# Kernel tuning notes

Hardware: AMD Instinct MI355X
Metric: run time of the kernel (lower is better)

The kernel has to match this reference:

```python
import jax, jax.numpy as jnp
import numpy as np

N, E, H, T = 50000, 100000, 512, 6  # nodes, edges, hidden_size, num_edge_types


def setup_inputs() -> dict:
    key = jax.random.key(0)
    ks = jax.random.split(key, 14)
    xav = 1.0 / np.sqrt(H)
    return {
        "statement_embeddings": jax.random.normal(ks[0], (N, H), jnp.float32),
        "source_indices": jax.random.randint(ks[1], (E,), 0, N, dtype=jnp.int32),
        "dest_indices": jax.random.randint(ks[2], (E,), 0, N, dtype=jnp.int32),
        "edge_types": jax.random.randint(ks[3], (E,), 0, T, dtype=jnp.int32),
        "num_nodes": N,
        "hidden_size": H,
        # edge_dense: Dense(features=6*H), xavier_uniform kernel, tiny-normal bias
        "W_edge": jax.random.uniform(ks[4], (H, T * H), jnp.float32, -1.0, 1.0) * np.sqrt(6.0 / (H + T * H)),
        "b_edge": jax.random.normal(ks[5], (T * H,), jnp.float32) * 1e-6,
        # GRUCell params (flax convention: input denses have bias; hidden r/z denses no bias; hidden n dense has bias)
        "W_ir": jax.random.normal(ks[6], (H, H), jnp.float32) * xav,
        "W_iz": jax.random.normal(ks[7], (H, H), jnp.float32) * xav,
        "W_in": jax.random.normal(ks[8], (H, H), jnp.float32) * xav,
        "b_ir": jnp.zeros((H,), jnp.float32),
        "b_iz": jnp.zeros((H,), jnp.float32),
        "b_in": jnp.zeros((H,), jnp.float32),
        "W_hr": jax.random.normal(ks[9], (H, H), jnp.float32) * xav,
        "W_hz": jax.random.normal(ks[10], (H, H), jnp.float32) * xav,
        "W_hn": jax.random.normal(ks[11], (H, H), jnp.float32) * xav,
        "b_hn": jnp.zeros((H,), jnp.float32),
    }


def reference(statement_embeddings, source_indices, dest_indices, edge_types,
              num_nodes, hidden_size,
              W_edge, b_edge,
              W_ir, W_iz, W_in, b_ir, b_iz, b_in,
              W_hr, W_hz, W_hn, b_hn):
    num_edge_types = 6
    # gather source node embeddings: [E, H]
    src = statement_embeddings[source_indices]
    # per-edge dense to all edge types: [E, T*H] -> [E, T, H]
    all_types = (src @ W_edge + b_edge).reshape(-1, num_edge_types, hidden_size)
    # select the slice for each edge's type: [E, H]
    msgs = jnp.take_along_axis(all_types, edge_types[:, None, None], axis=1)[:, 0, :]
    # scatter-add to destination nodes: [N, H]
    proposed = jax.ops.segment_sum(msgs, dest_indices, num_segments=num_nodes)
    # GRU update: inputs=proposed, carry=statement_embeddings
    h = statement_embeddings
    r = jax.nn.sigmoid(proposed @ W_ir + b_ir + h @ W_hr)
    z = jax.nn.sigmoid(proposed @ W_iz + b_iz + h @ W_hz)
    n = jnp.tanh(proposed @ W_in + b_in + r * (h @ W_hn + b_hn))
    return (1.0 - z) * n + z * h
```

## Files before the change

kernel.cpp:

```cpp
#include <hip/hip_runtime.h>
#include <hip/hip_bf16.h>
#include <math.h>

#define H 512
#define NT 6
#define BM 64
#define BN 64
#define BK 32
#define LDW (BK + 8)

typedef short bf16x8 __attribute__((ext_vector_type(8)));
typedef float f32x4 __attribute__((ext_vector_type(4)));

__device__ __forceinline__ float sigmoidf_(float x) { return 1.0f / (1.0f + expf(-x)); }

__device__ __forceinline__ unsigned short f2bf(float f) {
    unsigned int u = __float_as_uint(f);
    u = (u + 0x7FFF + ((u >> 16) & 1)) >> 16;
    return (unsigned short)u;
}

__global__ void hist_kernel(const int* __restrict__ etype, int E, int* __restrict__ meta) {
    __shared__ int lh[NT];
    if (threadIdx.x < NT) lh[threadIdx.x] = 0;
    __syncthreads();
    int i = blockIdx.x * blockDim.x + threadIdx.x;
    if (i < E) atomicAdd(&lh[etype[i]], 1);
    __syncthreads();
    if (threadIdx.x < NT) {
        int c = lh[threadIdx.x];
        if (c) atomicAdd(&meta[threadIdx.x], c);
    }
}

__global__ void prefix_kernel(int* __restrict__ meta) {
    if (threadIdx.x == 0 && blockIdx.x == 0) {
        int acc = 0;
        for (int t = 0; t < NT; ++t) {
            meta[8 + t]  = acc;
            meta[16 + t] = acc;
            acc += ((meta[t] + BM - 1) / BM) * BM;
        }
        meta[8 + NT] = acc;
    }
}

__global__ void scatter_perm_kernel(const int* __restrict__ etype, int E,
                                    int* __restrict__ meta, int* __restrict__ perm) {
    __shared__ int lcount[NT];
    __shared__ int lbase[NT];
    const int tid = threadIdx.x;
    if (tid < NT) lcount[tid] = 0;
    __syncthreads();
    int i = blockIdx.x * blockDim.x + tid;
    int t = 0, rank = 0;
    if (i < E) {
        t = etype[i];
        rank = atomicAdd(&lcount[t], 1);
    }
    __syncthreads();
    if (tid < NT) {
        int c = lcount[tid];
        lbase[tid] = c ? atomicAdd(&meta[16 + tid], c) : 0;
    }
    __syncthreads();
    if (i < E) perm[lbase[t] + rank] = i;
}

__global__ void conv_bf16_kernel(const float* __restrict__ in, unsigned short* __restrict__ out, int n4) {
    int i = blockIdx.x * blockDim.x + threadIdx.x;
    if (i < n4) {
        float4 v = ((const float4*)in)[i];
        ushort4 o;
        o.x = f2bf(v.x); o.y = f2bf(v.y); o.z = f2bf(v.z); o.w = f2bf(v.w);
        ((ushort4*)out)[i] = o;
    }
}

__global__ void conv_gru_w_kernel(const float* __restrict__ Wir, const float* __restrict__ Wiz,
                                  const float* __restrict__ Win, const float* __restrict__ Whr,
                                  const float* __restrict__ Whz, const float* __restrict__ Whn,
                                  unsigned short* __restrict__ Brt, unsigned short* __restrict__ Bzt,
                                  unsigned short* __restrict__ Bnit, unsigned short* __restrict__ Bnht) {
    int idx = blockIdx.x * blockDim.x + threadIdx.x;
    if (idx >= 512 * 1024) return;
    int n = idx >> 10;
    int k = idx & 1023;
    int kk = k & 511;
    const float* wr = (k < 512) ? Wir : Whr;
    const float* wz = (k < 512) ? Wiz : Whz;
    Brt[idx] = f2bf(wr[kk * H + n]);
    Bzt[idx] = f2bf(wz[kk * H + n]);
    if (k < 512) Bnit[n * H + k]  = f2bf(Win[k * H + n]);
    else         Bnht[n * H + kk] = f2bf(Whn[kk * H + n]);
}

__global__ void conv_edge_w_kernel(const float* __restrict__ W_edge, unsigned short* __restrict__ WeT) {
    int idx = blockIdx.x * blockDim.x + threadIdx.x;
    if (idx >= 3072 * 512) return;
    int n = idx >> 9;
    int k = idx & 511;
    WeT[idx] = f2bf(W_edge[(size_t)k * (NT * H) + n]);
}

__global__ __launch_bounds__(256)
void edge_msg_mfma(const unsigned short* __restrict__ emb_bf,
                   const int* __restrict__ src_idx,
                   const int* __restrict__ dst_idx,
                   const float* __restrict__ b_edge,
                   const unsigned short* __restrict__ WeT,
                   const int* __restrict__ meta,
                   const int* __restrict__ perm,
                   float* __restrict__ proposed)
{
    __shared__ short As[BM][LDW];
    __shared__ short Bs[BN][LDW];
    __shared__ int ls_src[BM];
    __shared__ int ls_dst[BM];

    const int rowBase = blockIdx.y * BM;
    if (rowBase >= meta[8 + NT]) return;
    int t = 0;
    while (rowBase >= meta[8 + t + 1]) ++t;

    const int colBase = blockIdx.x * BN;
    const int tid = threadIdx.x;

    if (tid < BM) {
        int e = perm[rowBase + tid];
        int s = -1, d = -1;
        if (e >= 0) { s = src_idx[e] * H; d = dst_idx[e] * H; }
        ls_src[tid] = s;
        ls_dst[tid] = d;
    }
    __syncthreads();

    const int sRow = tid >> 2;
    const int sK   = (tid & 3) * 8;
    const int lane = tid & 63;
    const int wave = tid >> 6;
    const int wm = (wave >> 1) * 32;
    const int wn = (wave & 1) * 32;
    const int q = lane >> 4;
    const int r = lane & 15;

    f32x4 acc[2][2];
    #pragma unroll
    for (int i = 0; i < 2; ++i)
        #pragma unroll
        for (int j = 0; j < 2; ++j) acc[i][j] = (f32x4){0.f, 0.f, 0.f, 0.f};

    const int sA = ls_src[sRow];
    const size_t bRowBase = ((size_t)(t * H + colBase + sRow)) * H;

    for (int k0 = 0; k0 < H; k0 += BK) {
        uint4 av = make_uint4(0, 0, 0, 0);
        if (sA >= 0) av = *(const uint4*)&emb_bf[(size_t)sA + k0 + sK];
        *(uint4*)&As[sRow][sK] = av;
        *(uint4*)&Bs[sRow][sK] = *(const uint4*)&WeT[bRowBase + k0 + sK];
        __syncthreads();
        #pragma unroll
        for (int i = 0; i < 2; ++i) {
            bf16x8 a = *(const bf16x8*)&As[wm + i * 16 + r][q * 8];
            #pragma unroll
            for (int j = 0; j < 2; ++j) {
                bf16x8 b = *(const bf16x8*)&Bs[wn + j * 16 + r][q * 8];
                acc[i][j] = __builtin_amdgcn_mfma_f32_16x16x32_bf16(a, b, acc[i][j], 0, 0, 0);
            }
        }
        __syncthreads();
    }

    #pragma unroll
    for (int i = 0; i < 2; ++i) {
        #pragma unroll
        for (int reg = 0; reg < 4; ++reg) {
            int rowL = wm + i * 16 + q * 4 + reg;
            int d = ls_dst[rowL];
            if (d < 0) continue;
            #pragma unroll
            for (int j = 0; j < 2; ++j) {
                int col = colBase + wn + j * 16 + r;
                atomicAdd(&proposed[(size_t)d + col], acc[i][j][reg] + b_edge[t * H + col]);
            }
        }
    }
}

__global__ __launch_bounds__(256)
void gru_mfma(const unsigned short* __restrict__ prop_bf,
              const unsigned short* __restrict__ emb_bf,
              const float* __restrict__ emb_f32,
              const unsigned short* __restrict__ Brt,
              const unsigned short* __restrict__ Bzt,
              const unsigned short* __restrict__ Bnit,
              const unsigned short* __restrict__ Bnht,
              const float* __restrict__ bir, const float* __restrict__ biz,
              const float* __restrict__ bin, const float* __restrict__ bhn,
              float* __restrict__ out, int N)
{
    __shared__ short As[BM][LDW];
    __shared__ short Brs[BN][LDW];
    __shared__ short Bzs[BN][LDW];
    __shared__ short Bns[BN][LDW];

    const int rowBase = blockIdx.y * BM;
    const int colBase = blockIdx.x * BN;
    const int tid = threadIdx.x;
    const int sRow = tid >> 2;
    const int sK   = (tid & 3) * 8;
    const int lane = tid & 63;
    const int wave = tid >> 6;
    const int wm = (wave >> 1) * 32;
    const int wn = (wave & 1) * 32;
    const int q = lane >> 4;
    const int r = lane & 15;

    const int aRow = rowBase + sRow;
    const bool aValid = aRow < N;

    f32x4 accR[2][2], accZ[2][2], accNI[2][2], accNH[2][2];
    #pragma unroll
    for (int i = 0; i < 2; ++i)
        #pragma unroll
        for (int j = 0; j < 2; ++j) {
            accR[i][j] = (f32x4){0.f, 0.f, 0.f, 0.f};
            accZ[i][j] = accR[i][j];
            accNI[i][j] = accR[i][j];
            accNH[i][j] = accR[i][j];
        }

    const size_t bRow = (size_t)(colBase + sRow);

    for (int k0 = 0; k0 < 2 * H; k0 += BK) {
        const bool half = (k0 >= H);
        const int kk = half ? (k0 - H) : k0;
        const unsigned short* Asrc = half ? emb_bf : prop_bf;
        uint4 av = make_uint4(0, 0, 0, 0);
        if (aValid) av = *(const uint4*)&Asrc[(size_t)aRow * H + kk + sK];
        *(uint4*)&As[sRow][sK] = av;
        *(uint4*)&Brs[sRow][sK] = *(const uint4*)&Brt[bRow * 1024 + k0 + sK];
        *(uint4*)&Bzs[sRow][sK] = *(const uint4*)&Bzt[bRow * 1024 + k0 + sK];
        const unsigned short* Bn = half ? Bnht : Bnit;
        *(uint4*)&Bns[sRow][sK] = *(const uint4*)&Bn[bRow * H + kk + sK];
        __syncthreads();

        #pragma unroll
        for (int i = 0; i < 2; ++i) {
            bf16x8 a = *(const bf16x8*)&As[wm + i * 16 + r][q * 8];
            #pragma unroll
            for (int j = 0; j < 2; ++j) {
                bf16x8 br = *(const bf16x8*)&Brs[wn + j * 16 + r][q * 8];
                bf16x8 bz = *(const bf16x8*)&Bzs[wn + j * 16 + r][q * 8];
                bf16x8 bn = *(const bf16x8*)&Bns[wn + j * 16 + r][q * 8];
                accR[i][j] = __builtin_amdgcn_mfma_f32_16x16x32_bf16(a, br, accR[i][j], 0, 0, 0);
                accZ[i][j] = __builtin_amdgcn_mfma_f32_16x16x32_bf16(a, bz, accZ[i][j], 0, 0, 0);
                if (half) accNH[i][j] = __builtin_amdgcn_mfma_f32_16x16x32_bf16(a, bn, accNH[i][j], 0, 0, 0);
                else      accNI[i][j] = __builtin_amdgcn_mfma_f32_16x16x32_bf16(a, bn, accNI[i][j], 0, 0, 0);
            }
        }
        __syncthreads();
    }

    #pragma unroll
    for (int i = 0; i < 2; ++i) {
        #pragma unroll
        for (int reg = 0; reg < 4; ++reg) {
            int row = rowBase + wm + i * 16 + q * 4 + reg;
            if (row >= N) continue;
            #pragma unroll
            for (int j = 0; j < 2; ++j) {
                int col = colBase + wn + j * 16 + r;
                float rg = sigmoidf_(accR[i][j][reg] + bir[col]);
                float zg = sigmoidf_(accZ[i][j][reg] + biz[col]);
                float ng = tanhf(accNI[i][j][reg] + bin[col] + rg * (accNH[i][j][reg] + bhn[col]));
                float h = emb_f32[(size_t)row * H + col];
                out[(size_t)row * H + col] = (1.0f - zg) * ng + zg * h;
            }
        }
    }
}

extern "C" void kernel_launch(void* const* d_in, const int* in_sizes, int n_in,
                              void* d_out, int out_size, void* d_ws, size_t ws_size,
                              hipStream_t stream) {
    const float* emb     = (const float*)d_in[0];
    const int*   src_idx = (const int*)d_in[1];
    const int*   dst_idx = (const int*)d_in[2];
    const int*   etype   = (const int*)d_in[3];
    const float* W_edge  = (const float*)d_in[6];
    const float* b_edge  = (const float*)d_in[7];
    const float* Wir = (const float*)d_in[8];
    const float* Wiz = (const float*)d_in[9];
    const float* Win = (const float*)d_in[10];
    const float* bir = (const float*)d_in[11];
    const float* biz = (const float*)d_in[12];
    const float* bin = (const float*)d_in[13];
    const float* Whr = (const float*)d_in[14];
    const float* Whz = (const float*)d_in[15];
    const float* Whn = (const float*)d_in[16];
    const float* bhn = (const float*)d_in[17];

    const int E = in_sizes[1];
    const int N = in_sizes[0] / H;
    const int NH = N * H;

    char* ws = (char*)d_ws;
    float*          proposed = (float*)ws;                       ws += (size_t)NH * 4;
    unsigned short* prop_bf  = (unsigned short*)ws;              ws += (size_t)NH * 2;
    unsigned short* emb_bf   = (unsigned short*)ws;              ws += (size_t)NH * 2;
    unsigned short* Brt      = (unsigned short*)ws;              ws += 512 * 1024 * 2;
    unsigned short* Bzt      = (unsigned short*)ws;              ws += 512 * 1024 * 2;
    unsigned short* Bnit     = (unsigned short*)ws;              ws += 512 * 512 * 2;
    unsigned short* Bnht     = (unsigned short*)ws;              ws += 512 * 512 * 2;
    unsigned short* WeT      = (unsigned short*)ws;              ws += 3072 * 512 * 2;
    int*            meta     = (int*)ws;                         ws += 32 * 4;
    int*            perm     = (int*)ws;
    const int maxRowTiles = (E + BM - 1) / BM + NT;

    hipMemsetAsync(proposed, 0, (size_t)NH * 4, stream);
    hipMemsetAsync(meta, 0, 32 * 4, stream);
    hipMemsetAsync(perm, 0xFF, (size_t)maxRowTiles * BM * 4, stream);

    const int n4 = NH / 4;
    conv_bf16_kernel<<<(n4 + 255) / 256, 256, 0, stream>>>(emb, emb_bf, n4);
    conv_gru_w_kernel<<<(512 * 1024 + 255) / 256, 256, 0, stream>>>(
        Wir, Wiz, Win, Whr, Whz, Whn, Brt, Bzt, Bnit, Bnht);
    conv_edge_w_kernel<<<(3072 * 512 + 255) / 256, 256, 0, stream>>>(W_edge, WeT);

    hist_kernel<<<(E + 255) / 256, 256, 0, stream>>>(etype, E, meta);
    prefix_kernel<<<1, 64, 0, stream>>>(meta);
    scatter_perm_kernel<<<(E + 255) / 256, 256, 0, stream>>>(etype, E, meta, perm);

    dim3 egrid(H / BN, maxRowTiles);
    edge_msg_mfma<<<egrid, 256, 0, stream>>>(emb_bf, src_idx, dst_idx, b_edge, WeT,
                                             meta, perm, proposed);

    conv_bf16_kernel<<<(n4 + 255) / 256, 256, 0, stream>>>(proposed, prop_bf, n4);

    dim3 ggrid(H / BN, (N + BM - 1) / BM);
    gru_mfma<<<ggrid, 256, 0, stream>>>(prop_bf, emb_bf, emb, Brt, Bzt, Bnit, Bnht,
                                        bir, biz, bin, bhn, (float*)d_out, N);
}
```

Baseline: 912.3 us.

## Replace atomic scatter with CSR segment reduce and async LDS loads in GEMMs

Builds a destination-sorted CSR layout (node histogram, multi-pass scan, slot assignment) so each edge message is written as bf16 to a unique slot. A segment-reduce kernel then sums messages per node directly into bf16, replacing the fp32 atomic scatter and the separate conversion pass. Both MFMA GEMMs now stage tiles with global_load_lds async copies in a per-wave fragment layout, loading a full 64-row block per k-step. This adds a large E×H message buffer, several extra small launches, and bf16 rounding of messages. The GRU kernel no longer bounds-checks rows when loading A, so it can read past the end when N is not a multiple of 64.

```diff
diff --git a/kernel.cpp b/kernel.cpp
--- a/kernel.cpp
+++ b/kernel.cpp
@@ -6,8 +6,6 @@
 #define NT 6
 #define BM 64
 #define BN 64
-#define BK 32
-#define LDW (BK + 8)
 
 typedef short bf16x8 __attribute__((ext_vector_type(8)));
 typedef float f32x4 __attribute__((ext_vector_type(4)));
@@ -18,6 +16,15 @@
     unsigned int u = __float_as_uint(f);
     u = (u + 0x7FFF + ((u >> 16) & 1)) >> 16;
     return (unsigned short)u;
+}
+__device__ __forceinline__ float bf2f(unsigned short s) {
+    unsigned int u = ((unsigned int)s) << 16;
+    return __uint_as_float(u);
+}
+
+__device__ __forceinline__ void async16(const unsigned short* g, short* l) {
+    __builtin_amdgcn_global_load_lds((const __attribute__((address_space(1))) void*)g,
+                                     (__attribute__((address_space(3))) void*)l, 16, 0, 0);
 }
 
 __global__ void hist_kernel(const int* __restrict__ etype, int E, int* __restrict__ meta) {
@@ -65,6 +72,59 @@
     }
     __syncthreads();
     if (i < E) perm[lbase[t] + rank] = i;
+}
+
+__global__ void node_hist_kernel(const int* __restrict__ dst, int E, int* __restrict__ cnt) {
+    int i = blockIdx.x * blockDim.x + threadIdx.x;
+    if (i < E) atomicAdd(&cnt[dst[i]], 1);
+}
+
+__global__ void scan1_kernel(const int* __restrict__ cnt, int n,
+                             int* __restrict__ nodeStart, int* __restrict__ partials) {
+    __shared__ int sh[256];
+    const int tid = threadIdx.x;
+    const int base = blockIdx.x * 1024 + tid * 4;
+    int v[4];
+    int tsum = 0;
+    #pragma unroll
+    for (int j = 0; j < 4; ++j) { v[j] = (base + j < n) ? cnt[base + j] : 0; tsum += v[j]; }
+    sh[tid] = tsum;
+    __syncthreads();
+    for (int ofs = 1; ofs < 256; ofs <<= 1) {
+        int add = (tid >= ofs) ? sh[tid - ofs] : 0;
+        __syncthreads();
+        sh[tid] += add;
+        __syncthreads();
+    }
+    int run = sh[tid] - tsum;
+    #pragma unroll
+    for (int j = 0; j < 4; ++j) {
+        if (base + j < n) nodeStart[base + j] = run;
+        run += v[j];
+    }
+    if (tid == 255) partials[blockIdx.x] = sh[255];
+}
+
+__global__ void scan2_kernel(int* __restrict__ partials, int nB, int* __restrict__ nodeStart, int n) {
+    if (threadIdx.x == 0 && blockIdx.x == 0) {
+        int acc = 0;
+        for (int b = 0; b < nB; ++b) { int t = partials[b]; partials[b] = acc; acc += t; }
+        nodeStart[n] = acc;
+    }
+}
+
+__global__ void scan3_kernel(int* __restrict__ nodeStart, const int* __restrict__ partials, int n) {
+    int i = blockIdx.x * blockDim.x + threadIdx.x;
+    if (i < n) nodeStart[i] += partials[i >> 10];
+}
+
+__global__ void slot_kernel(const int* __restrict__ dst, int E, const int* __restrict__ nodeStart,
+                            int* __restrict__ cursor, int* __restrict__ destSlot) {
+    int i = blockIdx.x * blockDim.x + threadIdx.x;
+    if (i < E) {
+        int d = dst[i];
+        destSlot[i] = nodeStart[d] + atomicAdd(&cursor[d], 1);
+    }
 }
 
 __global__ void conv_bf16_kernel(const float* __restrict__ in, unsigned short* __restrict__ out, int n4) {
@@ -104,19 +164,19 @@
 }
 
 __global__ __launch_bounds__(256)
-void edge_msg_mfma(const unsigned short* __restrict__ emb_bf,
-                   const int* __restrict__ src_idx,
-                   const int* __restrict__ dst_idx,
-                   const float* __restrict__ b_edge,
-                   const unsigned short* __restrict__ WeT,
-                   const int* __restrict__ meta,
-                   const int* __restrict__ perm,
-                   float* __restrict__ proposed)
+void edge_msg_mfma2(const unsigned short* __restrict__ emb_bf,
+                    const int* __restrict__ src_idx,
+                    const float* __restrict__ b_edge,
+                    const unsigned short* __restrict__ WeT,
+                    const int* __restrict__ meta,
+                    const int* __restrict__ perm,
+                    const int* __restrict__ destSlot,
+                    unsigned short* __restrict__ msgbuf)
 {
-    __shared__ short As[BM][LDW];
-    __shared__ short Bs[BN][LDW];
-    __shared__ int ls_src[BM];
-    __shared__ int ls_dst[BM];
+    __shared__ __align__(16) short lds[8 * 512];
+    __shared__ __align__(16) short Cs[64][72];
+    __shared__ int ls_slot[BM];
+    __shared__ int ls_srcb[BM];
 
     const int rowBase = blockIdx.y * BM;
     if (rowBase >= meta[8 + NT]) return;
@@ -125,24 +185,29 @@
 
     const int colBase = blockIdx.x * BN;
     const int tid = threadIdx.x;
-
     if (tid < BM) {
         int e = perm[rowBase + tid];
-        int s = -1, d = -1;
-        if (e >= 0) { s = src_idx[e] * H; d = dst_idx[e] * H; }
-        ls_src[tid] = s;
-        ls_dst[tid] = d;
-    }
-    __syncthreads();
-
-    const int sRow = tid >> 2;
-    const int sK   = (tid & 3) * 8;
+        ls_slot[tid] = (e >= 0) ? destSlot[e] : -1;
+        ls_srcb[tid] = (e >= 0) ? src_idx[e] * H : 0;
+    }
+    __syncthreads();
+
     const int lane = tid & 63;
-    const int wave = tid >> 6;
-    const int wm = (wave >> 1) * 32;
-    const int wn = (wave & 1) * 32;
+    const int wv = tid >> 6;
+    const int r = lane & 15;
     const int q = lane >> 4;
-    const int r = lane & 15;
+    const int wm = (wv >> 1) * 32;
+    const int wn = (wv & 1) * 32;
+
+    const unsigned short* pg[2];
+    #pragma unroll
+    for (int s = 0; s < 2; ++s) {
+        int grp = wv * 2 + s;
+        if (grp < 4) pg[s] = emb_bf + (size_t)ls_srcb[grp * 16 + r] + q * 8;
+        else         pg[s] = WeT + ((size_t)(t * H + colBase + (grp - 4) * 16 + r)) * H + q * 8;
+    }
+    short* ld0 = &lds[(wv * 2) * 512];
+    short* ld1 = &lds[(wv * 2 + 1) * 512];
 
     f32x4 acc[2][2];
     #pragma unroll
@@ -150,74 +215,88 @@
         #pragma unroll
         for (int j = 0; j < 2; ++j) acc[i][j] = (f32x4){0.f, 0.f, 0.f, 0.f};
 
-    const int sA = ls_src[sRow];
-    const size_t bRowBase = ((size_t)(t * H + colBase + sRow)) * H;
-
-    for (int k0 = 0; k0 < H; k0 += BK) {
-        uint4 av = make_uint4(0, 0, 0, 0);
-        if (sA >= 0) av = *(const uint4*)&emb_bf[(size_t)sA + k0 + sK];
-        *(uint4*)&As[sRow][sK] = av;
-        *(uint4*)&Bs[sRow][sK] = *(const uint4*)&WeT[bRowBase + k0 + sK];
+    for (int ks = 0; ks < 16; ++ks) {
+        async16(pg[0], ld0);
+        async16(pg[1], ld1);
+        pg[0] += 32; pg[1] += 32;
         __syncthreads();
-        #pragma unroll
-        for (int i = 0; i < 2; ++i) {
-            bf16x8 a = *(const bf16x8*)&As[wm + i * 16 + r][q * 8];
-            #pragma unroll
-            for (int j = 0; j < 2; ++j) {
-                bf16x8 b = *(const bf16x8*)&Bs[wn + j * 16 + r][q * 8];
-                acc[i][j] = __builtin_amdgcn_mfma_f32_16x16x32_bf16(a, b, acc[i][j], 0, 0, 0);
-            }
-        }
+        bf16x8 a0 = *(const bf16x8*)&lds[(wm / 16 + 0) * 512 + lane * 8];
+        bf16x8 a1 = *(const bf16x8*)&lds[(wm / 16 + 1) * 512 + lane * 8];
+        bf16x8 b0 = *(const bf16x8*)&lds[(4 + wn / 16 + 0) * 512 + lane * 8];
+        bf16x8 b1 = *(const bf16x8*)&lds[(4 + wn / 16 + 1) * 512 + lane * 8];
+        acc[0][0] = __builtin_amdgcn_mfma_f32_16x16x32_bf16(a0, b0, acc[0][0], 0, 0, 0);
+        acc[0][1] = __builtin_amdgcn_mfma_f32_16x16x32_bf16(a0, b1, acc[0][1], 0, 0, 0);
+        acc[1][0] = __builtin_amdgcn_mfma_f32_16x16x32_bf16(a1, b0, acc[1][0], 0, 0, 0);
+        acc[1][1] = __builtin_amdgcn_mfma_f32_16x16x32_bf16(a1, b1, acc[1][1], 0, 0, 0);
         __syncthreads();
     }
 
-    #pragma unroll
-    for (int i = 0; i < 2; ++i) {
+    float bias0 = b_edge[t * H + colBase + wn + r];
+    float bias1 = b_edge[t * H + colBase + wn + 16 + r];
+    #pragma unroll
+    for (int i = 0; i < 2; ++i)
         #pragma unroll
         for (int reg = 0; reg < 4; ++reg) {
-            int rowL = wm + i * 16 + q * 4 + reg;
-            int d = ls_dst[rowL];
-            if (d < 0) continue;
-            #pragma unroll
-            for (int j = 0; j < 2; ++j) {
-                int col = colBase + wn + j * 16 + r;
-                atomicAdd(&proposed[(size_t)d + col], acc[i][j][reg] + b_edge[t * H + col]);
-            }
-        }
-    }
+            int row = wm + i * 16 + q * 4 + reg;
+            Cs[row][wn + r]      = (short)f2bf(acc[i][0][reg] + bias0);
+            Cs[row][wn + 16 + r] = (short)f2bf(acc[i][1][reg] + bias1);
+        }
+    __syncthreads();
+
+    int row = tid >> 2;
+    int cc = (tid & 3) * 16;
+    int slot = ls_slot[row];
+    if (slot >= 0) {
+        uint4* dst0 = (uint4*)&msgbuf[(size_t)slot * H + colBase + cc];
+        dst0[0] = *(const uint4*)&Cs[row][cc];
+        dst0[1] = *(const uint4*)&Cs[row][cc + 8];
+    }
+}
+
+__global__ void segreduce_kernel(const unsigned short* __restrict__ msgbuf,
+                                 const int* __restrict__ nodeStart,
+                                 unsigned short* __restrict__ prop_bf, int N) {
+    int idx = blockIdx.x * blockDim.x + threadIdx.x;
+    if (idx >= N * 64) return;
+    int node = idx >> 6;
+    int cg = (idx & 63) * 8;
+    int s0 = nodeStart[node], s1 = nodeStart[node + 1];
+    float acc[8] = {0.f, 0.f, 0.f, 0.f, 0.f, 0.f, 0.f, 0.f};
+    for (int s = s0; s < s1; ++s) {
+        uint4 v = *(const uint4*)&msgbuf[(size_t)s * H + cg];
+        const unsigned short* u = (const unsigned short*)&v;
+        #pragma unroll
+        for (int j = 0; j < 8; ++j) acc[j] += bf2f(u[j]);
+    }
+    unsigned short o[8];
+    #pragma unroll
+    for (int j = 0; j < 8; ++j) o[j] = f2bf(acc[j]);
+    *(uint4*)&prop_bf[(size_t)node * H + cg] = *(const uint4*)o;
 }
 
 __global__ __launch_bounds__(256)
-void gru_mfma(const unsigned short* __restrict__ prop_bf,
-              const unsigned short* __restrict__ emb_bf,
-              const float* __restrict__ emb_f32,
-              const unsigned short* __restrict__ Brt,
-              const unsigned short* __restrict__ Bzt,
-              const unsigned short* __restrict__ Bnit,
-              const unsigned short* __restrict__ Bnht,
-              const float* __restrict__ bir, const float* __restrict__ biz,
-              const float* __restrict__ bin, const float* __restrict__ bhn,
-              float* __restrict__ out, int N)
+void gru_mfma2(const unsigned short* __restrict__ prop_bf,
+               const unsigned short* __restrict__ emb_bf,
+               const float* __restrict__ emb_f32,
+               const unsigned short* __restrict__ Brt,
+               const unsigned short* __restrict__ Bzt,
+               const unsigned short* __restrict__ Bnit,
+               const unsigned short* __restrict__ Bnht,
+               const float* __restrict__ bir, const float* __restrict__ biz,
+               const float* __restrict__ bin, const float* __restrict__ bhn,
+               float* __restrict__ out, int N)
 {
-    __shared__ short As[BM][LDW];
-    __shared__ short Brs[BN][LDW];
-    __shared__ short Bzs[BN][LDW];
-    __shared__ short Bns[BN][LDW];
-
+    __shared__ __align__(16) short lds[4 * 2048];
+
+    const int tid = threadIdx.x;
+    const int lane = tid & 63;
+    const int wv = tid >> 6;
+    const int r = lane & 15;
+    const int q = lane >> 4;
     const int rowBase = blockIdx.y * BM;
     const int colBase = blockIdx.x * BN;
-    const int tid = threadIdx.x;
-    const int sRow = tid >> 2;
-    const int sK   = (tid & 3) * 8;
-    const int lane = tid & 63;
-    const int wave = tid >> 6;
-    const int wm = (wave >> 1) * 32;
-    const int wn = (wave & 1) * 32;
-    const int q = lane >> 4;
-    const int r = lane & 15;
-
-    const int aRow = rowBase + sRow;
-    const bool aValid = aRow < N;
+    const int wm = (wv >> 1) * 32;
+    const int wn = (wv & 1) * 32;
 
     f32x4 accR[2][2], accZ[2][2], accNI[2][2], accNH[2][2];
     #pragma unroll
@@ -230,36 +309,63 @@
             accNH[i][j] = accR[i][j];
         }
 
-    const size_t bRow = (size_t)(colBase + sRow);
-
-    for (int k0 = 0; k0 < 2 * H; k0 += BK) {
-        const bool half = (k0 >= H);
-        const int kk = half ? (k0 - H) : k0;
-        const unsigned short* Asrc = half ? emb_bf : prop_bf;
-        uint4 av = make_uint4(0, 0, 0, 0);
-        if (aValid) av = *(const uint4*)&Asrc[(size_t)aRow * H + kk + sK];
-        *(uint4*)&As[sRow][sK] = av;
-        *(uint4*)&Brs[sRow][sK] = *(const uint4*)&Brt[bRow * 1024 + k0 + sK];
-        *(uint4*)&Bzs[sRow][sK] = *(const uint4*)&Bzt[bRow * 1024 + k0 + sK];
-        const unsigned short* Bn = half ? Bnht : Bnit;
-        *(uint4*)&Bns[sRow][sK] = *(const uint4*)&Bn[bRow * H + kk + sK];
-        __syncthreads();
-
-        #pragma unroll
-        for (int i = 0; i < 2; ++i) {
-            bf16x8 a = *(const bf16x8*)&As[wm + i * 16 + r][q * 8];
-            #pragma unroll
-            for (int j = 0; j < 2; ++j) {
-                bf16x8 br = *(const bf16x8*)&Brs[wn + j * 16 + r][q * 8];
-                bf16x8 bz = *(const bf16x8*)&Bzs[wn + j * 16 + r][q * 8];
-                bf16x8 bn = *(const bf16x8*)&Bns[wn + j * 16 + r][q * 8];
-                accR[i][j] = __builtin_amdgcn_mfma_f32_16x16x32_bf16(a, br, accR[i][j], 0, 0, 0);
-                accZ[i][j] = __builtin_amdgcn_mfma_f32_16x16x32_bf16(a, bz, accZ[i][j], 0, 0, 0);
-                if (half) accNH[i][j] = __builtin_amdgcn_mfma_f32_16x16x32_bf16(a, bn, accNH[i][j], 0, 0, 0);
-                else      accNI[i][j] = __builtin_amdgcn_mfma_f32_16x16x32_bf16(a, bn, accNI[i][j], 0, 0, 0);
+    short* ldsT = &lds[wv * 2048];
+
+    for (int half = 0; half < 2; ++half) {
+        const unsigned short* pg[4];
+        if (wv == 0) {
+            const unsigned short* s = half ? emb_bf : prop_bf;
+            #pragma unroll
+            for (int g = 0; g < 4; ++g)
+                pg[g] = s + (size_t)(rowBase + g * 16 + r) * H + q * 8;
+        } else if (wv == 1) {
+            #pragma unroll
+            for (int g = 0; g < 4; ++g)
+                pg[g] = Brt + (size_t)(colBase + g * 16 + r) * 1024 + half * 512 + q * 8;
+        } else if (wv == 2) {
+            #pragma unroll
+            for (int g = 0; g < 4; ++g)
+                pg[g] = Bzt + (size_t)(colBase + g * 16 + r) * 1024 + half * 512 + q * 8;
+        } else {
+            const unsigned short* s = half ? Bnht : Bnit;
+            #pragma unroll
+            for (int g = 0; g < 4; ++g)
+                pg[g] = s + (size_t)(colBase + g * 16 + r) * H + q * 8;
+        }
+
+        f32x4 (&accN)[2][2] = half ? accNH : accNI;
+
+        for (int ks = 0; ks < 16; ++ks) {
+            #pragma unroll
+            for (int g = 0; g < 4; ++g) {
+                async16(pg[g], ldsT + g * 512);
+                pg[g] += 32;
             }
-        }
-        __syncthreads();
+            __syncthreads();
+
+            bf16x8 a0 = *(const bf16x8*)&lds[0 * 2048 + (wm / 16 + 0) * 512 + lane * 8];
+            bf16x8 a1 = *(const bf16x8*)&lds[0 * 2048 + (wm / 16 + 1) * 512 + lane * 8];
+            bf16x8 br0 = *(const bf16x8*)&lds[1 * 2048 + (wn / 16 + 0) * 512 + lane * 8];
+            bf16x8 br1 = *(const bf16x8*)&lds[1 * 2048 + (wn / 16 + 1) * 512 + lane * 8];
+            bf16x8 bz0 = *(const bf16x8*)&lds[2 * 2048 + (wn / 16 + 0) * 512 + lane * 8];
+            bf16x8 bz1 = *(const bf16x8*)&lds[2 * 2048 + (wn / 16 + 1) * 512 + lane * 8];
+            bf16x8 bn0 = *(const bf16x8*)&lds[3 * 2048 + (wn / 16 + 0) * 512 + lane * 8];
+            bf16x8 bn1 = *(const bf16x8*)&lds[3 * 2048 + (wn / 16 + 1) * 512 + lane * 8];
+
+            accR[0][0] = __builtin_amdgcn_mfma_f32_16x16x32_bf16(a0, br0, accR[0][0], 0, 0, 0);
+            accR[0][1] = __builtin_amdgcn_mfma_f32_16x16x32_bf16(a0, br1, accR[0][1], 0, 0, 0);
+            accR[1][0] = __builtin_amdgcn_mfma_f32_16x16x32_bf16(a1, br0, accR[1][0], 0, 0, 0);
+            accR[1][1] = __builtin_amdgcn_mfma_f32_16x16x32_bf16(a1, br1, accR[1][1], 0, 0, 0);
+            accZ[0][0] = __builtin_amdgcn_mfma_f32_16x16x32_bf16(a0, bz0, accZ[0][0], 0, 0, 0);
+            accZ[0][1] = __builtin_amdgcn_mfma_f32_16x16x32_bf16(a0, bz1, accZ[0][1], 0, 0, 0);
+            accZ[1][0] = __builtin_amdgcn_mfma_f32_16x16x32_bf16(a1, bz0, accZ[1][0], 0, 0, 0);
+            accZ[1][1] = __builtin_amdgcn_mfma_f32_16x16x32_bf16(a1, bz1, accZ[1][1], 0, 0, 0);
+            accN[0][0] = __builtin_amdgcn_mfma_f32_16x16x32_bf16(a0, bn0, accN[0][0], 0, 0, 0);
+            accN[0][1] = __builtin_amdgcn_mfma_f32_16x16x32_bf16(a0, bn1, accN[0][1], 0, 0, 0);
+            accN[1][0] = __builtin_amdgcn_mfma_f32_16x16x32_bf16(a1, bn0, accN[1][0], 0, 0, 0);
+            accN[1][1] = __builtin_amdgcn_mfma_f32_16x16x32_bf16(a1, bn1, accN[1][1], 0, 0, 0);
+            __syncthreads();
+        }
     }
 
     #pragma unroll
@@ -304,23 +410,29 @@
     const int E = in_sizes[1];
     const int N = in_sizes[0] / H;
     const int NH = N * H;
+    const int maxRowTiles = (E + BM - 1) / BM + NT;
 
     char* ws = (char*)d_ws;
-    float*          proposed = (float*)ws;                       ws += (size_t)NH * 4;
-    unsigned short* prop_bf  = (unsigned short*)ws;              ws += (size_t)NH * 2;
-    unsigned short* emb_bf   = (unsigned short*)ws;              ws += (size_t)NH * 2;
-    unsigned short* Brt      = (unsigned short*)ws;              ws += 512 * 1024 * 2;
-    unsigned short* Bzt      = (unsigned short*)ws;              ws += 512 * 1024 * 2;
-    unsigned short* Bnit     = (unsigned short*)ws;              ws += 512 * 512 * 2;
-    unsigned short* Bnht     = (unsigned short*)ws;              ws += 512 * 512 * 2;
-    unsigned short* WeT      = (unsigned short*)ws;              ws += 3072 * 512 * 2;
-    int*            meta     = (int*)ws;                         ws += 32 * 4;
-    int*            perm     = (int*)ws;
-    const int maxRowTiles = (E + BM - 1) / BM + NT;
-
-    hipMemsetAsync(proposed, 0, (size_t)NH * 4, stream);
+    unsigned short* prop_bf  = (unsigned short*)ws;  ws += (size_t)NH * 2;
+    unsigned short* emb_bf   = (unsigned short*)ws;  ws += (size_t)NH * 2;
+    unsigned short* msgbuf   = (unsigned short*)ws;  ws += (size_t)E * H * 2;
+    unsigned short* Brt      = (unsigned short*)ws;  ws += 512 * 1024 * 2;
+    unsigned short* Bzt      = (unsigned short*)ws;  ws += 512 * 1024 * 2;
+    unsigned short* Bnit     = (unsigned short*)ws;  ws += 512 * 512 * 2;
+    unsigned short* Bnht     = (unsigned short*)ws;  ws += 512 * 512 * 2;
+    unsigned short* WeT      = (unsigned short*)ws;  ws += 3072 * 512 * 2;
+    int* meta      = (int*)ws;  ws += 32 * 4;
+    int* typePerm  = (int*)ws;  ws += (size_t)maxRowTiles * BM * 4;
+    int* nodeCnt   = (int*)ws;  ws += (size_t)N * 4;
+    int* nodeStart = (int*)ws;  ws += ((size_t)N + 4) * 4;
+    int* cursor    = (int*)ws;  ws += (size_t)N * 4;
+    int* partials  = (int*)ws;  ws += 64 * 4;
+    int* destSlot  = (int*)ws;
+
     hipMemsetAsync(meta, 0, 32 * 4, stream);
-    hipMemsetAsync(perm, 0xFF, (size_t)maxRowTiles * BM * 4, stream);
+    hipMemsetAsync(typePerm, 0xFF, (size_t)maxRowTiles * BM * 4, stream);
+    hipMemsetAsync(nodeCnt, 0, (size_t)N * 4, stream);
+    hipMemsetAsync(cursor, 0, (size_t)N * 4, stream);
 
     const int n4 = NH / 4;
     conv_bf16_kernel<<<(n4 + 255) / 256, 256, 0, stream>>>(emb, emb_bf, n4);
@@ -330,15 +442,22 @@
 
     hist_kernel<<<(E + 255) / 256, 256, 0, stream>>>(etype, E, meta);
     prefix_kernel<<<1, 64, 0, stream>>>(meta);
-    scatter_perm_kernel<<<(E + 255) / 256, 256, 0, stream>>>(etype, E, meta, perm);
+    scatter_perm_kernel<<<(E + 255) / 256, 256, 0, stream>>>(etype, E, meta, typePerm);
+
+    node_hist_kernel<<<(E + 255) / 256, 256, 0, stream>>>(dst_idx, E, nodeCnt);
+    const int nB = (N + 1023) / 1024;
+    scan1_kernel<<<nB, 256, 0, stream>>>(nodeCnt, N, nodeStart, partials);
+    scan2_kernel<<<1, 64, 0, stream>>>(partials, nB, nodeStart, N);
+    scan3_kernel<<<(N + 255) / 256, 256, 0, stream>>>(nodeStart, partials, N);
+    slot_kernel<<<(E + 255) / 256, 256, 0, stream>>>(dst_idx, E, nodeStart, cursor, destSlot);
 
     dim3 egrid(H / BN, maxRowTiles);
-    edge_msg_mfma<<<egrid, 256, 0, stream>>>(emb_bf, src_idx, dst_idx, b_edge, WeT,
-                                             meta, perm, proposed);
-
-    conv_bf16_kernel<<<(n4 + 255) / 256, 256, 0, stream>>>(proposed, prop_bf, n4);
+    edge_msg_mfma2<<<egrid, 256, 0, stream>>>(emb_bf, src_idx, b_edge, WeT,
+                                              meta, typePerm, destSlot, msgbuf);
+
+    segreduce_kernel<<<((size_t)N * 64 + 255) / 256, 256, 0, stream>>>(msgbuf, nodeStart, prop_bf, N);
 
     dim3 ggrid(H / BN, (N + BM - 1) / BM);
-    gru_mfma<<<ggrid, 256, 0, stream>>>(prop_bf, emb_bf, emb, Brt, Bzt, Bnit, Bnht,
-                                        bir, biz, bin, bhn, (float*)d_out, N);
-}
+    gru_mfma2<<<ggrid, 256, 0, stream>>>(prop_bf, emb_bf, emb, Brt, Bzt, Bnit, Bnht,
+                                         bir, biz, bin, bhn, (float*)d_out, N);
+}
```

Result: slower. 940.7 us (+3.1%).
